# Performance work log

Measured on AMD Instinct MI355X. Metric: run time of the kernel, lower is better.

The kernel has to match this reference:

```python
import jax, jax.numpy as jnp
import numpy as np

D_MODEL = 1024
NUM_HEADS = 16
SCALE = 1.0 / np.sqrt(D_MODEL // NUM_HEADS)  # matches sqrt(d_model // num_heads)


def setup_inputs() -> dict:
    key = jax.random.key(0)
    ks = jax.random.split(key, 7)
    B, S, D = 4, 2048, D_MODEL
    std = 1.0 / np.sqrt(D)
    return {
        "x": jax.random.normal(ks[0], (B, S, D), dtype=jnp.float32),
        "Wq": jax.random.normal(ks[1], (D, D), dtype=jnp.float32) * std,
        "bq": jnp.zeros((D,), dtype=jnp.float32),
        "Wk": jax.random.normal(ks[2], (D, D), dtype=jnp.float32) * std,
        "bk": jnp.zeros((D,), dtype=jnp.float32),
        "Wv": jax.random.normal(ks[3], (D, D), dtype=jnp.float32) * std,
        "bv": jnp.zeros((D,), dtype=jnp.float32),
    }


def reference(x, Wq, bq, Wk, bk, Wv, bv):
    # QKV projections (nn.Linear: x @ W^T + b; here W stored as [in, out] already)
    Q = x @ Wq + bq  # [B, S, D]
    K = x @ Wk + bk
    V = x @ Wv + bv
    scores = jnp.einsum("bsd,btd->bst", Q, K) * SCALE  # [B, S, S]
    S_len = x.shape[1]
    causal = jnp.tril(jnp.ones((S_len, S_len), dtype=bool))
    scores = jnp.where(causal, scores, -jnp.inf)
    attn = jax.nn.softmax(scores, axis=-1)
    return jnp.einsum("bst,btd->bsd", attn, V)
```

## Files before the change

kernel.cpp:

```cpp
#include <hip/hip_runtime.h>
#include <hip/hip_bf16.h>
#include <cstdint>

#define D_MODEL 1024
#define SEQ     2048
#define SCALE   0.125f
#define P_ELEMS 2228224

typedef __attribute__((ext_vector_type(8))) _Float16 f16x8;
typedef __attribute__((ext_vector_type(8))) unsigned short u16x8;
typedef __attribute__((ext_vector_type(4))) float f32x4;

__device__ __forceinline__ unsigned short f2h(float f) {
  _Float16 h = (_Float16)f;
  return __builtin_bit_cast(unsigned short, h);
}
__device__ __forceinline__ float h2f(unsigned short u) {
  return (float)__builtin_bit_cast(_Float16, u);
}

__device__ __forceinline__ void gll16(const void* g, void* lds_p) {
  __builtin_amdgcn_global_load_lds(
      (const __attribute__((address_space(1))) unsigned int*)(uintptr_t)g,
      (__attribute__((address_space(3))) unsigned int*)(unsigned int)(uintptr_t)lds_p,
      16, 0, 0);
}

#define WAITV8 asm volatile("s_waitcnt vmcnt(8)" ::: "memory")
#define WAITV0 asm volatile("s_waitcnt vmcnt(0)" ::: "memory")
#define WAITL8 asm volatile("s_waitcnt lgkmcnt(8)" ::: "memory")
#define WAITL0 asm volatile("s_waitcnt lgkmcnt(0)" ::: "memory")
#define SCHEDB __builtin_amdgcn_sched_barrier(0)
#define BAR    __builtin_amdgcn_s_barrier()
#define PRIO1  __builtin_amdgcn_s_setprio(1)
#define PRIO0  __builtin_amdgcn_s_setprio(0)
#define MFMA16(a, b, c) __builtin_amdgcn_mfma_f32_16x16x32_f16(a, b, c, 0, 0, 0)

__device__ __forceinline__ void stage_tile(const unsigned short* gA, const unsigned short* gB,
                                           size_t sA, size_t sB,
                                           int k0, unsigned short* buf, int w, int lane) {
  int rl = lane >> 3;
  int sg = ((lane & 7) ^ rl) << 3;
#pragma unroll
  for (int j = 0; j < 4; j++) {
    int c = w * 4 + j;
    int row = c * 8 + rl;
    gll16(gA + (size_t)row * sA + k0 + sg, buf + c * 512);
    gll16(gB + (size_t)row * sB + k0 + sg, buf + 8192 + c * 512);
  }
}

__device__ __forceinline__ void gemm_core(const unsigned short* gA, const unsigned short* gB,
                                          size_t sA, size_t sB,
                                          unsigned short* lds0, unsigned short* lds1, int nt,
                                          int w, int lane, int wr, int wc, int l15, int l4,
                                          f32x4 acc[4][4]) {
  stage_tile(gA, gB, sA, sB, 0, lds0, w, lane);
  stage_tile(gA, gB, sA, sB, 64, lds1, w, lane);
  WAITV8; SCHEDB; BAR;
  for (int t = 0; t < nt; t++) {
    const unsigned short* buf = (t & 1) ? lds1 : lds0;
    const unsigned short* bA = buf;
    const unsigned short* bB = buf + 8192;
    f16x8 a0[4], b0[4], a1[4], b1[4];
#pragma unroll
    for (int m = 0; m < 4; m++) {
      int row = wr * 64 + m * 16 + l15, rs = row & 7;
      a0[m] = *(const f16x8*)(bA + row * 64 + ((l4 ^ rs) << 3));
    }
#pragma unroll
    for (int n = 0; n < 4; n++) {
      int row = wc * 64 + n * 16 + l15, rs = row & 7;
      b0[n] = *(const f16x8*)(bB + row * 64 + ((l4 ^ rs) << 3));
    }
#pragma unroll
    for (int m = 0; m < 4; m++) {
      int row = wr * 64 + m * 16 + l15, rs = row & 7;
      a1[m] = *(const f16x8*)(bA + row * 64 + (((4 + l4) ^ rs) << 3));
    }
#pragma unroll
    for (int n = 0; n < 4; n++) {
      int row = wc * 64 + n * 16 + l15, rs = row & 7;
      b1[n] = *(const f16x8*)(bB + row * 64 + (((4 + l4) ^ rs) << 3));
    }
    WAITL8; SCHEDB;
    PRIO1;
#pragma unroll
    for (int m = 0; m < 4; m++)
#pragma unroll
      for (int n = 0; n < 4; n++)
        acc[m][n] = MFMA16(a0[m], b0[n], acc[m][n]);
    PRIO0;
    WAITL0; SCHEDB; BAR;
    if (t + 2 < nt) stage_tile(gA, gB, sA, sB, (t + 2) * 64,
                               (unsigned short*)buf, w, lane);
    PRIO1;
#pragma unroll
    for (int m = 0; m < 4; m++)
#pragma unroll
      for (int n = 0; n < 4; n++)
        acc[m][n] = MFMA16(a1[m], b1[n], acc[m][n]);
    PRIO0;
    if (t + 2 < nt) { WAITV8; } else { WAITV0; }
    SCHEDB; BAR;
  }
}

__global__ __launch_bounds__(256) void cvt_fused(const float* __restrict__ x,
                                                 const float* __restrict__ W0,
                                                 const float* __restrict__ W1,
                                                 const float* __restrict__ W2,
                                                 unsigned short* __restrict__ xb,
                                                 unsigned short* __restrict__ wt) {
  __shared__ float t[32][33];
  int bid = blockIdx.x;
  int tid = threadIdx.x;
  if (bid < 4096) {
    int i = bid * 256 + tid;
    const float4* p = (const float4*)x + (size_t)i * 2;
    float4 a = p[0], b = p[1];
    u16x8 r;
    r[0] = f2h(a.x); r[1] = f2h(a.y); r[2] = f2h(a.z); r[3] = f2h(a.w);
    r[4] = f2h(b.x); r[5] = f2h(b.y); r[6] = f2h(b.z); r[7] = f2h(b.w);
    *((u16x8*)xb + i) = r;
  } else {
    int id = bid - 4096;
    int z = id >> 10, rem = id & 1023;
    int bx = rem & 31, by = rem >> 5;
    const float* W = (z == 0) ? W0 : (z == 1 ? W1 : W2);
    unsigned short* o = wt + (size_t)z * 1048576;
    int c0 = bx * 32, r0 = by * 32;
    int tx = tid & 31, ty = tid >> 5;
    for (int i = 0; i < 4; i++)
      t[ty + 8 * i][tx] = W[(size_t)(r0 + ty + 8 * i) * 1024 + c0 + tx];
    __syncthreads();
    for (int i = 0; i < 4; i++)
      o[(size_t)(c0 + ty + 8 * i) * 1024 + r0 + tx] = f2h(t[tx][ty + 8 * i]);
  }
}

__global__ __launch_bounds__(256) void qkv_gemm(const unsigned short* __restrict__ xb,
                                                const unsigned short* __restrict__ wt,
                                                const float* __restrict__ b0,
                                                const float* __restrict__ b1,
                                                const float* __restrict__ b2,
                                                unsigned short* __restrict__ Qp,
                                                unsigned short* __restrict__ Kp,
                                                unsigned short* __restrict__ vtp) {
  __shared__ unsigned short lds[2][16384];
  int m0 = blockIdx.x * 128;
  int n0 = blockIdx.y * 128;
  int z = n0 >> 10, nz = n0 & 1023;
  const unsigned short* gA = xb + (size_t)m0 * 1024;
  const unsigned short* gB = wt + (size_t)z * 1048576 + (size_t)nz * 1024;
  const float* bias = (z == 0) ? b0 : (z == 1 ? b1 : b2);
  int tid = threadIdx.x, lane = tid & 63, w = tid >> 6;
  int wr = w >> 1, wc = w & 1, l15 = lane & 15, l4 = lane >> 4;
  f32x4 acc[4][4] = {};
  gemm_core(gA, gB, 1024, 1024, &lds[0][0], &lds[1][0], 16, w, lane, wr, wc, l15, l4, acc);

  unsigned short* T = &lds[0][0];
  if (z < 2) {
    unsigned short* O = (z == 0) ? Qp : Kp;
#pragma unroll
    for (int m = 0; m < 4; m++)
#pragma unroll
      for (int n = 0; n < 4; n++) {
        int cl = wc * 64 + n * 16 + l15;
        float bv = bias[nz + cl];
#pragma unroll
        for (int r = 0; r < 4; r++) {
          int rl = wr * 64 + m * 16 + l4 * 4 + r;
          T[rl * 136 + cl] = f2h(acc[m][n][r] + bv);
        }
      }
    __syncthreads();
#pragma unroll
    for (int i = 0; i < 8; i++) {
      int idx = i * 256 + tid;
      int row = idx >> 4, ch = idx & 15;
      u16x8 v = *(const u16x8*)(T + row * 136 + ch * 8);
      *(u16x8*)(O + (size_t)(m0 + row) * 1024 + nz + ch * 8) = v;
    }
  } else {
#pragma unroll
    for (int m = 0; m < 4; m++)
#pragma unroll
      for (int n = 0; n < 4; n++) {
        int cl = wc * 64 + n * 16 + l15;
        float bv = bias[nz + cl];
#pragma unroll
        for (int r = 0; r < 4; r++) {
          int rl = wr * 64 + m * 16 + l4 * 4 + r;
          T[cl * 136 + rl] = f2h(acc[m][n][r] + bv);
        }
      }
    __syncthreads();
    int bidx = m0 >> 11, s0 = m0 & 2047;
#pragma unroll
    for (int i = 0; i < 8; i++) {
      int d = w * 32 + i * 4 + (lane >> 4);
      int ch = lane & 15;
      u16x8 v = *(const u16x8*)(T + d * 136 + ch * 8);
      *(u16x8*)(vtp + ((size_t)bidx * 1024 + nz + d) * 2048 + s0 + ch * 8) = v;
    }
  }
}

__global__ __launch_bounds__(256) void qk_scores(const unsigned short* __restrict__ Q,
                                                 const unsigned short* __restrict__ Kb,
                                                 unsigned short* __restrict__ sc) {
  __shared__ unsigned short lds[2][16384];
  int blk = blockIdx.x;
  int t0, ntile;
  if (blk < 32) { t0 = 480 + blk; ntile = 2; }
  else          { t0 = blk - 32;  ntile = 1; }
  int tid = threadIdx.x, lane = tid & 63, w = tid >> 6;
  int wr = w >> 1, wc = w & 1, l15 = lane & 15, l4 = lane >> 4;
  for (int u = 0; u < ntile; u++) {
    int ti = t0 + u * 32;
    int b = ti / 136, i = ti % 136;
    int qt = (int)((sqrtf(8.f * i + 1.f) - 1.f) * 0.5f);
    while ((qt + 1) * (qt + 2) / 2 <= i) qt++;
    while (qt * (qt + 1) / 2 > i) qt--;
    int kt = i - qt * (qt + 1) / 2;
    int Wspan = (qt + 1) << 7;
    const unsigned short* gA = Q  + ((size_t)b * 2048 + qt * 128) * 1024;
    const unsigned short* gB = Kb + ((size_t)b * 2048 + kt * 128) * 1024;
    unsigned short* outp = sc + (size_t)b * P_ELEMS + (size_t)16384 * (qt * (qt + 1) / 2);
    f32x4 acc[4][4] = {};
    gemm_core(gA, gB, 1024, 1024, &lds[0][0], &lds[1][0], 16, w, lane, wr, wc, l15, l4, acc);
    unsigned short* T = &lds[0][0];
#pragma unroll
    for (int m = 0; m < 4; m++)
#pragma unroll
      for (int n = 0; n < 4; n++) {
        int cl = wc * 64 + n * 16 + l15;
        int kv = kt * 128 + cl;
#pragma unroll
        for (int r = 0; r < 4; r++) {
          int rl = wr * 64 + m * 16 + l4 * 4 + r;
          int srow = qt * 128 + rl;
          float v = acc[m][n][r] * SCALE;
          if (kv > srow) v = -30000.f;
          T[rl * 136 + cl] = f2h(v);
        }
      }
    __syncthreads();
#pragma unroll
    for (int i2 = 0; i2 < 8; i2++) {
      int idx = i2 * 256 + tid;
      int row = idx >> 4, ch = idx & 15;
      u16x8 v = *(const u16x8*)(T + row * 136 + ch * 8);
      *(u16x8*)(outp + (size_t)row * Wspan + kt * 128 + ch * 8) = v;
    }
    __syncthreads();
  }
}

__global__ __launch_bounds__(256) void softmax_row(const unsigned short* __restrict__ sc,
                                                   unsigned short* __restrict__ pb) {
  int base = blockIdx.x * 4;
  int b = base >> 11, sl0 = base & 2047;
  int w = threadIdx.x >> 6, lane = threadIdx.x & 63;
  int sl = sl0 + w;
  int qt = sl >> 7;
  int Wspan = (qt + 1) << 7;
  size_t rb = (size_t)b * P_ELEMS + (size_t)16384 * (qt * (qt + 1) / 2) + (size_t)(sl & 127) * Wspan;
  const u16x8* src = (const u16x8*)(sc + rb);
  int nc = Wspan >> 3;
  bool h0 = lane < nc, h1 = lane + 64 < nc, h2 = lane + 128 < nc, h3 = lane + 192 < nc;
  float v0[8], v1[8], v2[8], v3[8];
  float mx = -1e30f;
  if (h0) { u16x8 r = src[lane];
#pragma unroll
    for (int j = 0; j < 8; j++) { v0[j] = h2f(r[j]); mx = fmaxf(mx, v0[j]); } }
  if (h1) { u16x8 r = src[lane + 64];
#pragma unroll
    for (int j = 0; j < 8; j++) { v1[j] = h2f(r[j]); mx = fmaxf(mx, v1[j]); } }
  if (h2) { u16x8 r = src[lane + 128];
#pragma unroll
    for (int j = 0; j < 8; j++) { v2[j] = h2f(r[j]); mx = fmaxf(mx, v2[j]); } }
  if (h3) { u16x8 r = src[lane + 192];
#pragma unroll
    for (int j = 0; j < 8; j++) { v3[j] = h2f(r[j]); mx = fmaxf(mx, v3[j]); } }
  for (int off = 1; off < 64; off <<= 1) mx = fmaxf(mx, __shfl_xor(mx, off, 64));
  float s = 0.f;
  if (h0) {
#pragma unroll
    for (int j = 0; j < 8; j++) { v0[j] = __expf(v0[j] - mx); s += v0[j]; } }
  if (h1) {
#pragma unroll
    for (int j = 0; j < 8; j++) { v1[j] = __expf(v1[j] - mx); s += v1[j]; } }
  if (h2) {
#pragma unroll
    for (int j = 0; j < 8; j++) { v2[j] = __expf(v2[j] - mx); s += v2[j]; } }
  if (h3) {
#pragma unroll
    for (int j = 0; j < 8; j++) { v3[j] = __expf(v3[j] - mx); s += v3[j]; } }
  for (int off = 1; off < 64; off <<= 1) s += __shfl_xor(s, off, 64);
  float inv = 1.f / s;
  u16x8* dst = (u16x8*)(pb + rb);
  if (h0) { u16x8 o;
#pragma unroll
    for (int j = 0; j < 8; j++) o[j] = f2h(v0[j] * inv);
    dst[lane] = o; }
  if (h1) { u16x8 o;
#pragma unroll
    for (int j = 0; j < 8; j++) o[j] = f2h(v1[j] * inv);
    dst[lane + 64] = o; }
  if (h2) { u16x8 o;
#pragma unroll
    for (int j = 0; j < 8; j++) o[j] = f2h(v2[j] * inv);
    dst[lane + 128] = o; }
  if (h3) { u16x8 o;
#pragma unroll
    for (int j = 0; j < 8; j++) o[j] = f2h(v3[j] * inv);
    dst[lane + 192] = o; }
}

__global__ __launch_bounds__(256) void pv_gemm(const unsigned short* __restrict__ pb,
                                               const unsigned short* __restrict__ vtp,
                                               float* __restrict__ outp) {
  __shared__ unsigned short lds[2][16384];
  int bx = blockIdx.x;
  int n0 = blockIdx.y * 128;
  int bz = blockIdx.z;
  int qt = (bz & 2) ? (15 - bx) : bx;
  int b = bz;
  int tid = threadIdx.x, lane = tid & 63, w = tid >> 6;
  int wr = w >> 1, wc = w & 1, l15 = lane & 15, l4 = lane >> 4;
  const unsigned short* gB = vtp + (size_t)b * 1024 * 2048 + (size_t)n0 * 2048;
  int Wspan = (qt + 1) << 7;
  const unsigned short* gA = pb + (size_t)b * P_ELEMS + (size_t)16384 * (qt * (qt + 1) / 2);
  float* O = outp + ((size_t)b * 2048 + qt * 128) * 1024;
  f32x4 acc[4][4] = {};
  gemm_core(gA, gB, Wspan, 2048, &lds[0][0], &lds[1][0], 2 * (qt + 1),
            w, lane, wr, wc, l15, l4, acc);
  float* Tf = (float*)&lds[0][0];
#pragma unroll
  for (int m = 0; m < 4; m++)
#pragma unroll
    for (int n = 0; n < 4; n++) {
      int cl = wc * 64 + n * 16 + l15;
#pragma unroll
      for (int r = 0; r < 4; r++) {
        int rl = wr * 64 + m * 16 + l4 * 4 + r;
        int cc = cl >> 2;
        int sw = (((cc ^ (rl & 7)) << 2) | (cl & 3));
        Tf[rl * 128 + sw] = acc[m][n][r];
      }
    }
  __syncthreads();
#pragma unroll
  for (int i = 0; i < 16; i++) {
    int idx = i * 256 + tid;
    int row = idx >> 5, ch = idx & 31;
    float4 val = *(const float4*)&Tf[row * 128 + ((ch ^ (row & 7)) << 2)];
    *(float4*)&O[(size_t)row * 1024 + n0 + ch * 4] = val;
  }
}

extern "C" void kernel_launch(void* const* d_in, const int* in_sizes, int n_in,
                              void* d_out, int out_size, void* d_ws, size_t ws_size,
                              hipStream_t stream) {
  const float* x  = (const float*)d_in[0];
  const float* Wq = (const float*)d_in[1];
  const float* bq = (const float*)d_in[2];
  const float* Wk = (const float*)d_in[3];
  const float* bk = (const float*)d_in[4];
  const float* Wv = (const float*)d_in[5];
  const float* bv = (const float*)d_in[6];
  float* out = (float*)d_out;

  unsigned short* ws  = (unsigned short*)d_ws;
  unsigned short* wt  = ws;
  unsigned short* Qp  = ws + 3145728;
  unsigned short* Kp  = ws + 11534336;
  unsigned short* vtp = ws + 19922944;
  unsigned short* sc  = ws + 28311552;
  unsigned short* pb  = ws + 37224448;
  unsigned short* xb  = (unsigned short*)d_out;

  cvt_fused<<<7168, 256, 0, stream>>>(x, Wq, Wk, Wv, xb, wt);
  qkv_gemm<<<dim3(64, 24), 256, 0, stream>>>(xb, wt, bq, bk, bv, Qp, Kp, vtp);
  qk_scores<<<512, 256, 0, stream>>>(Qp, Kp, sc);
  softmax_row<<<2048, 256, 0, stream>>>(sc, pb);
  pv_gemm<<<dim3(16, 8, 4), 256, 0, stream>>>(pb, vtp, out);
}
```

Baseline: 149.7 us.

## Switch GEMMs to 32x32x16 MFMA and fuse V projection into scores kernel

Replaces the 16x16x32 MFMA tiles with 32x32x16 MFMA in the shared GEMM core, so each wave issues fewer, larger matrix instructions and needs fewer LDS fragment loads per k-step. It also moves the V projection out of the QKV GEMM into the scores kernel as extra blocks. The scores tiles and the V projection tiles then run concurrently, which should fill the machine better and removes one launch-level dependency. The accumulator row mapping changes for the new MFMA layout, which risks register pressure and different epilogue bank conflicts.

```diff
diff --git a/kernel.cpp b/kernel.cpp
--- a/kernel.cpp
+++ b/kernel.cpp
@@ -9,7 +9,7 @@
 
 typedef __attribute__((ext_vector_type(8))) _Float16 f16x8;
 typedef __attribute__((ext_vector_type(8))) unsigned short u16x8;
-typedef __attribute__((ext_vector_type(4))) float f32x4;
+typedef __attribute__((ext_vector_type(16))) float f32x16;
 
 __device__ __forceinline__ unsigned short f2h(float f) {
   _Float16 h = (_Float16)f;
@@ -34,7 +34,7 @@
 #define BAR    __builtin_amdgcn_s_barrier()
 #define PRIO1  __builtin_amdgcn_s_setprio(1)
 #define PRIO0  __builtin_amdgcn_s_setprio(0)
-#define MFMA16(a, b, c) __builtin_amdgcn_mfma_f32_16x16x32_f16(a, b, c, 0, 0, 0)
+#define MFMA32(a, b, c) __builtin_amdgcn_mfma_f32_32x32x16_f16(a, b, c, 0, 0, 0)
 
 __device__ __forceinline__ void stage_tile(const unsigned short* gA, const unsigned short* gB,
                                            size_t sA, size_t sB,
@@ -52,59 +52,65 @@
 
 __device__ __forceinline__ void gemm_core(const unsigned short* gA, const unsigned short* gB,
                                           size_t sA, size_t sB,
-                                          unsigned short* lds0, unsigned short* lds1, int nt,
-                                          int w, int lane, int wr, int wc, int l15, int l4,
-                                          f32x4 acc[4][4]) {
+                                          unsigned short* lds0, unsigned short* lds1, int ntk,
+                                          int w, int lane, int wr, int wc, int l31, int l5,
+                                          f32x16 acc[2][2]) {
   stage_tile(gA, gB, sA, sB, 0, lds0, w, lane);
   stage_tile(gA, gB, sA, sB, 64, lds1, w, lane);
   WAITV8; SCHEDB; BAR;
-  for (int t = 0; t < nt; t++) {
-    const unsigned short* buf = (t & 1) ? lds1 : lds0;
+  int rA0 = wr * 64 + l31,      qA0 = rA0 & 7;
+  int rA1 = wr * 64 + 32 + l31, qA1 = rA1 & 7;
+  int rB0 = wc * 64 + l31,      qB0 = rB0 & 7;
+  int rB1 = wc * 64 + 32 + l31, qB1 = rB1 & 7;
+  for (int t = 0; t < ntk; t++) {
+    unsigned short* buf = (t & 1) ? lds1 : lds0;
     const unsigned short* bA = buf;
     const unsigned short* bB = buf + 8192;
-    f16x8 a0[4], b0[4], a1[4], b1[4];
-#pragma unroll
-    for (int m = 0; m < 4; m++) {
-      int row = wr * 64 + m * 16 + l15, rs = row & 7;
-      a0[m] = *(const f16x8*)(bA + row * 64 + ((l4 ^ rs) << 3));
-    }
-#pragma unroll
-    for (int n = 0; n < 4; n++) {
-      int row = wc * 64 + n * 16 + l15, rs = row & 7;
-      b0[n] = *(const f16x8*)(bB + row * 64 + ((l4 ^ rs) << 3));
-    }
-#pragma unroll
-    for (int m = 0; m < 4; m++) {
-      int row = wr * 64 + m * 16 + l15, rs = row & 7;
-      a1[m] = *(const f16x8*)(bA + row * 64 + (((4 + l4) ^ rs) << 3));
-    }
-#pragma unroll
-    for (int n = 0; n < 4; n++) {
-      int row = wc * 64 + n * 16 + l15, rs = row & 7;
-      b1[n] = *(const f16x8*)(bB + row * 64 + (((4 + l4) ^ rs) << 3));
+    f16x8 a[2][4], b[2][4];
+#pragma unroll
+    for (int ks = 0; ks < 2; ks++) {
+      int s = (ks << 1) | l5;
+      a[0][ks] = *(const f16x8*)(bA + rA0 * 64 + ((s ^ qA0) << 3));
+      a[1][ks] = *(const f16x8*)(bA + rA1 * 64 + ((s ^ qA1) << 3));
+      b[0][ks] = *(const f16x8*)(bB + rB0 * 64 + ((s ^ qB0) << 3));
+      b[1][ks] = *(const f16x8*)(bB + rB1 * 64 + ((s ^ qB1) << 3));
+    }
+    SCHEDB;
+#pragma unroll
+    for (int ks = 2; ks < 4; ks++) {
+      int s = (ks << 1) | l5;
+      a[0][ks] = *(const f16x8*)(bA + rA0 * 64 + ((s ^ qA0) << 3));
+      a[1][ks] = *(const f16x8*)(bA + rA1 * 64 + ((s ^ qA1) << 3));
+      b[0][ks] = *(const f16x8*)(bB + rB0 * 64 + ((s ^ qB0) << 3));
+      b[1][ks] = *(const f16x8*)(bB + rB1 * 64 + ((s ^ qB1) << 3));
     }
     WAITL8; SCHEDB;
     PRIO1;
 #pragma unroll
-    for (int m = 0; m < 4; m++)
-#pragma unroll
-      for (int n = 0; n < 4; n++)
-        acc[m][n] = MFMA16(a0[m], b0[n], acc[m][n]);
+    for (int ks = 0; ks < 2; ks++)
+#pragma unroll
+      for (int mt = 0; mt < 2; mt++)
+#pragma unroll
+        for (int nq = 0; nq < 2; nq++)
+          acc[mt][nq] = MFMA32(a[mt][ks], b[nq][ks], acc[mt][nq]);
     PRIO0;
     WAITL0; SCHEDB; BAR;
-    if (t + 2 < nt) stage_tile(gA, gB, sA, sB, (t + 2) * 64,
-                               (unsigned short*)buf, w, lane);
+    if (t + 2 < ntk) stage_tile(gA, gB, sA, sB, (t + 2) * 64, buf, w, lane);
     PRIO1;
 #pragma unroll
-    for (int m = 0; m < 4; m++)
-#pragma unroll
-      for (int n = 0; n < 4; n++)
-        acc[m][n] = MFMA16(a1[m], b1[n], acc[m][n]);
+    for (int ks = 2; ks < 4; ks++)
+#pragma unroll
+      for (int mt = 0; mt < 2; mt++)
+#pragma unroll
+        for (int nq = 0; nq < 2; nq++)
+          acc[mt][nq] = MFMA32(a[mt][ks], b[nq][ks], acc[mt][nq]);
     PRIO0;
-    if (t + 2 < nt) { WAITV8; } else { WAITV0; }
+    if (t + 2 < ntk) { WAITV8; } else { WAITV0; }
     SCHEDB; BAR;
   }
 }
+
+#define ACC_ROW(r, l5) (((r) & 3) + (((r) >> 2) << 3) + ((l5) << 2))
 
 __global__ __launch_bounds__(256) void cvt_fused(const float* __restrict__ x,
                                                  const float* __restrict__ W0,
@@ -143,56 +149,117 @@
                                                 const unsigned short* __restrict__ wt,
                                                 const float* __restrict__ b0,
                                                 const float* __restrict__ b1,
-                                                const float* __restrict__ b2,
                                                 unsigned short* __restrict__ Qp,
-                                                unsigned short* __restrict__ Kp,
-                                                unsigned short* __restrict__ vtp) {
+                                                unsigned short* __restrict__ Kp) {
   __shared__ unsigned short lds[2][16384];
   int m0 = blockIdx.x * 128;
   int n0 = blockIdx.y * 128;
   int z = n0 >> 10, nz = n0 & 1023;
   const unsigned short* gA = xb + (size_t)m0 * 1024;
   const unsigned short* gB = wt + (size_t)z * 1048576 + (size_t)nz * 1024;
-  const float* bias = (z == 0) ? b0 : (z == 1 ? b1 : b2);
+  const float* bias = z ? b1 : b0;
+  unsigned short* O = z ? Kp : Qp;
   int tid = threadIdx.x, lane = tid & 63, w = tid >> 6;
-  int wr = w >> 1, wc = w & 1, l15 = lane & 15, l4 = lane >> 4;
-  f32x4 acc[4][4] = {};
-  gemm_core(gA, gB, 1024, 1024, &lds[0][0], &lds[1][0], 16, w, lane, wr, wc, l15, l4, acc);
+  int wr = w >> 1, wc = w & 1, l31 = lane & 31, l5 = lane >> 5;
+  f32x16 acc[2][2] = {};
+  gemm_core(gA, gB, 1024, 1024, &lds[0][0], &lds[1][0], 16, w, lane, wr, wc, l31, l5, acc);
 
   unsigned short* T = &lds[0][0];
-  if (z < 2) {
-    unsigned short* O = (z == 0) ? Qp : Kp;
-#pragma unroll
-    for (int m = 0; m < 4; m++)
-#pragma unroll
-      for (int n = 0; n < 4; n++) {
-        int cl = wc * 64 + n * 16 + l15;
-        float bv = bias[nz + cl];
-#pragma unroll
-        for (int r = 0; r < 4; r++) {
-          int rl = wr * 64 + m * 16 + l4 * 4 + r;
-          T[rl * 136 + cl] = f2h(acc[m][n][r] + bv);
+#pragma unroll
+  for (int mt = 0; mt < 2; mt++)
+#pragma unroll
+    for (int nq = 0; nq < 2; nq++) {
+      int cl = wc * 64 + nq * 32 + l31;
+      float bvv = bias[nz + cl];
+#pragma unroll
+      for (int r = 0; r < 16; r++) {
+        int rl = wr * 64 + mt * 32 + ACC_ROW(r, l5);
+        T[rl * 136 + cl] = f2h(acc[mt][nq][r] + bvv);
+      }
+    }
+  __syncthreads();
+#pragma unroll
+  for (int i = 0; i < 8; i++) {
+    int idx = i * 256 + tid;
+    int row = idx >> 4, ch = idx & 15;
+    u16x8 v = *(const u16x8*)(T + row * 136 + ch * 8);
+    *(u16x8*)(O + (size_t)(m0 + row) * 1024 + nz + ch * 8) = v;
+  }
+}
+
+__global__ __launch_bounds__(256) void scores_v(const unsigned short* __restrict__ Q,
+                                                const unsigned short* __restrict__ Kb,
+                                                const unsigned short* __restrict__ xb,
+                                                const unsigned short* __restrict__ wt,
+                                                const float* __restrict__ bvf,
+                                                unsigned short* __restrict__ sc,
+                                                unsigned short* __restrict__ vtp) {
+  __shared__ unsigned short lds[2][16384];
+  int blk = blockIdx.x;
+  int tid = threadIdx.x, lane = tid & 63, w = tid >> 6;
+  int wr = w >> 1, wc = w & 1, l31 = lane & 31, l5 = lane >> 5;
+  if (blk < 512) {
+    int t0, ntile;
+    if (blk < 32) { t0 = 480 + blk; ntile = 2; }
+    else          { t0 = blk - 32;  ntile = 1; }
+    for (int u = 0; u < ntile; u++) {
+      int ti = t0 + u * 32;
+      int b = ti / 136, i = ti % 136;
+      int qt = (int)((sqrtf(8.f * i + 1.f) - 1.f) * 0.5f);
+      while ((qt + 1) * (qt + 2) / 2 <= i) qt++;
+      while (qt * (qt + 1) / 2 > i) qt--;
+      int kt = i - qt * (qt + 1) / 2;
+      int Wspan = (qt + 1) << 7;
+      const unsigned short* gA = Q  + ((size_t)b * 2048 + qt * 128) * 1024;
+      const unsigned short* gB = Kb + ((size_t)b * 2048 + kt * 128) * 1024;
+      unsigned short* outp = sc + (size_t)b * P_ELEMS + (size_t)16384 * (qt * (qt + 1) / 2);
+      f32x16 acc[2][2] = {};
+      gemm_core(gA, gB, 1024, 1024, &lds[0][0], &lds[1][0], 16, w, lane, wr, wc, l31, l5, acc);
+      unsigned short* T = &lds[0][0];
+#pragma unroll
+      for (int mt = 0; mt < 2; mt++)
+#pragma unroll
+        for (int nq = 0; nq < 2; nq++) {
+          int cl = wc * 64 + nq * 32 + l31;
+          int kv = kt * 128 + cl;
+#pragma unroll
+          for (int r = 0; r < 16; r++) {
+            int rl = wr * 64 + mt * 32 + ACC_ROW(r, l5);
+            int srow = qt * 128 + rl;
+            float v = acc[mt][nq][r] * SCALE;
+            if (kv > srow) v = -30000.f;
+            T[rl * 136 + cl] = f2h(v);
+          }
         }
+      __syncthreads();
+#pragma unroll
+      for (int i2 = 0; i2 < 8; i2++) {
+        int idx = i2 * 256 + tid;
+        int row = idx >> 4, ch = idx & 15;
+        u16x8 v = *(const u16x8*)(T + row * 136 + ch * 8);
+        *(u16x8*)(outp + (size_t)row * Wspan + kt * 128 + ch * 8) = v;
       }
-    __syncthreads();
-#pragma unroll
-    for (int i = 0; i < 8; i++) {
-      int idx = i * 256 + tid;
-      int row = idx >> 4, ch = idx & 15;
-      u16x8 v = *(const u16x8*)(T + row * 136 + ch * 8);
-      *(u16x8*)(O + (size_t)(m0 + row) * 1024 + nz + ch * 8) = v;
+      __syncthreads();
     }
   } else {
-#pragma unroll
-    for (int m = 0; m < 4; m++)
-#pragma unroll
-      for (int n = 0; n < 4; n++) {
-        int cl = wc * 64 + n * 16 + l15;
-        float bv = bias[nz + cl];
-#pragma unroll
-        for (int r = 0; r < 4; r++) {
-          int rl = wr * 64 + m * 16 + l4 * 4 + r;
-          T[cl * 136 + rl] = f2h(acc[m][n][r] + bv);
+    int id = blk - 512;
+    int m0 = (id & 63) * 128;
+    int n0v = (id >> 6) * 128;
+    const unsigned short* gA = xb + (size_t)m0 * 1024;
+    const unsigned short* gB = wt + (size_t)2 * 1048576 + (size_t)n0v * 1024;
+    f32x16 acc[2][2] = {};
+    gemm_core(gA, gB, 1024, 1024, &lds[0][0], &lds[1][0], 16, w, lane, wr, wc, l31, l5, acc);
+    unsigned short* T = &lds[0][0];
+#pragma unroll
+    for (int mt = 0; mt < 2; mt++)
+#pragma unroll
+      for (int nq = 0; nq < 2; nq++) {
+        int cl = wc * 64 + nq * 32 + l31;
+        float bvv = bvf[n0v + cl];
+#pragma unroll
+        for (int r = 0; r < 16; r++) {
+          int rl = wr * 64 + mt * 32 + ACC_ROW(r, l5);
+          T[cl * 136 + rl] = f2h(acc[mt][nq][r] + bvv);
         }
       }
     __syncthreads();
@@ -202,59 +269,8 @@
       int d = w * 32 + i * 4 + (lane >> 4);
       int ch = lane & 15;
       u16x8 v = *(const u16x8*)(T + d * 136 + ch * 8);
-      *(u16x8*)(vtp + ((size_t)bidx * 1024 + nz + d) * 2048 + s0 + ch * 8) = v;
-    }
-  }
-}
-
-__global__ __launch_bounds__(256) void qk_scores(const unsigned short* __restrict__ Q,
-                                                 const unsigned short* __restrict__ Kb,
-                                                 unsigned short* __restrict__ sc) {
-  __shared__ unsigned short lds[2][16384];
-  int blk = blockIdx.x;
-  int t0, ntile;
-  if (blk < 32) { t0 = 480 + blk; ntile = 2; }
-  else          { t0 = blk - 32;  ntile = 1; }
-  int tid = threadIdx.x, lane = tid & 63, w = tid >> 6;
-  int wr = w >> 1, wc = w & 1, l15 = lane & 15, l4 = lane >> 4;
-  for (int u = 0; u < ntile; u++) {
-    int ti = t0 + u * 32;
-    int b = ti / 136, i = ti % 136;
-    int qt = (int)((sqrtf(8.f * i + 1.f) - 1.f) * 0.5f);
-    while ((qt + 1) * (qt + 2) / 2 <= i) qt++;
-    while (qt * (qt + 1) / 2 > i) qt--;
-    int kt = i - qt * (qt + 1) / 2;
-    int Wspan = (qt + 1) << 7;
-    const unsigned short* gA = Q  + ((size_t)b * 2048 + qt * 128) * 1024;
-    const unsigned short* gB = Kb + ((size_t)b * 2048 + kt * 128) * 1024;
-    unsigned short* outp = sc + (size_t)b * P_ELEMS + (size_t)16384 * (qt * (qt + 1) / 2);
-    f32x4 acc[4][4] = {};
-    gemm_core(gA, gB, 1024, 1024, &lds[0][0], &lds[1][0], 16, w, lane, wr, wc, l15, l4, acc);
-    unsigned short* T = &lds[0][0];
-#pragma unroll
-    for (int m = 0; m < 4; m++)
-#pragma unroll
-      for (int n = 0; n < 4; n++) {
-        int cl = wc * 64 + n * 16 + l15;
-        int kv = kt * 128 + cl;
-#pragma unroll
-        for (int r = 0; r < 4; r++) {
-          int rl = wr * 64 + m * 16 + l4 * 4 + r;
-          int srow = qt * 128 + rl;
-          float v = acc[m][n][r] * SCALE;
-          if (kv > srow) v = -30000.f;
-          T[rl * 136 + cl] = f2h(v);
-        }
-      }
-    __syncthreads();
-#pragma unroll
-    for (int i2 = 0; i2 < 8; i2++) {
-      int idx = i2 * 256 + tid;
-      int row = idx >> 4, ch = idx & 15;
-      u16x8 v = *(const u16x8*)(T + row * 136 + ch * 8);
-      *(u16x8*)(outp + (size_t)row * Wspan + kt * 128 + ch * 8) = v;
-    }
-    __syncthreads();
+      *(u16x8*)(vtp + ((size_t)bidx * 1024 + n0v + d) * 2048 + s0 + ch * 8) = v;
+    }
   }
 }
 
@@ -329,26 +345,26 @@
   int qt = (bz & 2) ? (15 - bx) : bx;
   int b = bz;
   int tid = threadIdx.x, lane = tid & 63, w = tid >> 6;
-  int wr = w >> 1, wc = w & 1, l15 = lane & 15, l4 = lane >> 4;
+  int wr = w >> 1, wc = w & 1, l31 = lane & 31, l5 = lane >> 5;
   const unsigned short* gB = vtp + (size_t)b * 1024 * 2048 + (size_t)n0 * 2048;
   int Wspan = (qt + 1) << 7;
   const unsigned short* gA = pb + (size_t)b * P_ELEMS + (size_t)16384 * (qt * (qt + 1) / 2);
   float* O = outp + ((size_t)b * 2048 + qt * 128) * 1024;
-  f32x4 acc[4][4] = {};
+  f32x16 acc[2][2] = {};
   gemm_core(gA, gB, Wspan, 2048, &lds[0][0], &lds[1][0], 2 * (qt + 1),
-            w, lane, wr, wc, l15, l4, acc);
+            w, lane, wr, wc, l31, l5, acc);
   float* Tf = (float*)&lds[0][0];
 #pragma unroll
-  for (int m = 0; m < 4; m++)
-#pragma unroll
-    for (int n = 0; n < 4; n++) {
-      int cl = wc * 64 + n * 16 + l15;
-#pragma unroll
-      for (int r = 0; r < 4; r++) {
-        int rl = wr * 64 + m * 16 + l4 * 4 + r;
+  for (int mt = 0; mt < 2; mt++)
+#pragma unroll
+    for (int nq = 0; nq < 2; nq++) {
+      int cl = wc * 64 + nq * 32 + l31;
+#pragma unroll
+      for (int r = 0; r < 16; r++) {
+        int rl = wr * 64 + mt * 32 + ACC_ROW(r, l5);
         int cc = cl >> 2;
         int sw = (((cc ^ (rl & 7)) << 2) | (cl & 3));
-        Tf[rl * 128 + sw] = acc[m][n][r];
+        Tf[rl * 128 + sw] = acc[mt][nq][r];
       }
     }
   __syncthreads();
@@ -383,8 +399,8 @@
   unsigned short* xb  = (unsigned short*)d_out;
 
   cvt_fused<<<7168, 256, 0, stream>>>(x, Wq, Wk, Wv, xb, wt);
-  qkv_gemm<<<dim3(64, 24), 256, 0, stream>>>(xb, wt, bq, bk, bv, Qp, Kp, vtp);
-  qk_scores<<<512, 256, 0, stream>>>(Qp, Kp, sc);
+  qkv_gemm<<<dim3(64, 16), 256, 0, stream>>>(xb, wt, bq, bk, Qp, Kp);
+  scores_v<<<1024, 256, 0, stream>>>(Qp, Kp, xb, wt, bv, sc, vtp);
   softmax_row<<<2048, 256, 0, stream>>>(sc, pb);
   pv_gemm<<<dim3(16, 8, 4), 256, 0, stream>>>(pb, vtp, out);
 }
```

New measurement: 156.0 us. 1.04x slower.

## Move V projection into the QK-scores kernel to balance grid waves

Applied to the files above, without the earlier changes.

The V projection tiles are taken out of the QKV GEMM launch and run in the same launch as the causal QK^T score tiles, using a block-index split (first 512 blocks do scores, the next 512 compute V transposed). The QKV GEMM grid drops from 1536 to 1024 blocks and the scores kernel grows from 512 to 1024 blocks. The intent is to fill partial waves on the 256-CU device and overlap the independent V GEMM with the score GEMM, with the same total work. The combined kernel mixes two workload types, and placement of its blocks is left to the hardware scheduler.

```diff
diff --git a/kernel.cpp b/kernel.cpp
--- a/kernel.cpp
+++ b/kernel.cpp
@@ -143,56 +143,117 @@
                                                 const unsigned short* __restrict__ wt,
                                                 const float* __restrict__ b0,
                                                 const float* __restrict__ b1,
-                                                const float* __restrict__ b2,
                                                 unsigned short* __restrict__ Qp,
-                                                unsigned short* __restrict__ Kp,
-                                                unsigned short* __restrict__ vtp) {
+                                                unsigned short* __restrict__ Kp) {
   __shared__ unsigned short lds[2][16384];
   int m0 = blockIdx.x * 128;
   int n0 = blockIdx.y * 128;
   int z = n0 >> 10, nz = n0 & 1023;
   const unsigned short* gA = xb + (size_t)m0 * 1024;
   const unsigned short* gB = wt + (size_t)z * 1048576 + (size_t)nz * 1024;
-  const float* bias = (z == 0) ? b0 : (z == 1 ? b1 : b2);
+  const float* bias = z ? b1 : b0;
+  unsigned short* O = z ? Kp : Qp;
   int tid = threadIdx.x, lane = tid & 63, w = tid >> 6;
   int wr = w >> 1, wc = w & 1, l15 = lane & 15, l4 = lane >> 4;
   f32x4 acc[4][4] = {};
   gemm_core(gA, gB, 1024, 1024, &lds[0][0], &lds[1][0], 16, w, lane, wr, wc, l15, l4, acc);
 
   unsigned short* T = &lds[0][0];
-  if (z < 2) {
-    unsigned short* O = (z == 0) ? Qp : Kp;
+#pragma unroll
+  for (int m = 0; m < 4; m++)
+#pragma unroll
+    for (int n = 0; n < 4; n++) {
+      int cl = wc * 64 + n * 16 + l15;
+      float bv = bias[nz + cl];
+#pragma unroll
+      for (int r = 0; r < 4; r++) {
+        int rl = wr * 64 + m * 16 + l4 * 4 + r;
+        T[rl * 136 + cl] = f2h(acc[m][n][r] + bv);
+      }
+    }
+  __syncthreads();
+#pragma unroll
+  for (int i = 0; i < 8; i++) {
+    int idx = i * 256 + tid;
+    int row = idx >> 4, ch = idx & 15;
+    u16x8 v = *(const u16x8*)(T + row * 136 + ch * 8);
+    *(u16x8*)(O + (size_t)(m0 + row) * 1024 + nz + ch * 8) = v;
+  }
+}
+
+__global__ __launch_bounds__(256) void scores_v(const unsigned short* __restrict__ Q,
+                                                const unsigned short* __restrict__ Kb,
+                                                const unsigned short* __restrict__ xb,
+                                                const unsigned short* __restrict__ wt,
+                                                const float* __restrict__ bvf,
+                                                unsigned short* __restrict__ sc,
+                                                unsigned short* __restrict__ vtp) {
+  __shared__ unsigned short lds[2][16384];
+  int blk = blockIdx.x;
+  int tid = threadIdx.x, lane = tid & 63, w = tid >> 6;
+  int wr = w >> 1, wc = w & 1, l15 = lane & 15, l4 = lane >> 4;
+  if (blk < 512) {
+    int t0, ntile;
+    if (blk < 32) { t0 = 480 + blk; ntile = 2; }
+    else          { t0 = blk - 32;  ntile = 1; }
+    for (int u = 0; u < ntile; u++) {
+      int ti = t0 + u * 32;
+      int b = ti / 136, i = ti % 136;
+      int qt = (int)((sqrtf(8.f * i + 1.f) - 1.f) * 0.5f);
+      while ((qt + 1) * (qt + 2) / 2 <= i) qt++;
+      while (qt * (qt + 1) / 2 > i) qt--;
+      int kt = i - qt * (qt + 1) / 2;
+      int Wspan = (qt + 1) << 7;
+      const unsigned short* gA = Q  + ((size_t)b * 2048 + qt * 128) * 1024;
+      const unsigned short* gB = Kb + ((size_t)b * 2048 + kt * 128) * 1024;
+      unsigned short* outp = sc + (size_t)b * P_ELEMS + (size_t)16384 * (qt * (qt + 1) / 2);
+      f32x4 acc[4][4] = {};
+      gemm_core(gA, gB, 1024, 1024, &lds[0][0], &lds[1][0], 16, w, lane, wr, wc, l15, l4, acc);
+      unsigned short* T = &lds[0][0];
+#pragma unroll
+      for (int m = 0; m < 4; m++)
+#pragma unroll
+        for (int n = 0; n < 4; n++) {
+          int cl = wc * 64 + n * 16 + l15;
+          int kv = kt * 128 + cl;
+#pragma unroll
+          for (int r = 0; r < 4; r++) {
+            int rl = wr * 64 + m * 16 + l4 * 4 + r;
+            int srow = qt * 128 + rl;
+            float v = acc[m][n][r] * SCALE;
+            if (kv > srow) v = -30000.f;
+            T[rl * 136 + cl] = f2h(v);
+          }
+        }
+      __syncthreads();
+#pragma unroll
+      for (int i2 = 0; i2 < 8; i2++) {
+        int idx = i2 * 256 + tid;
+        int row = idx >> 4, ch = idx & 15;
+        u16x8 v = *(const u16x8*)(T + row * 136 + ch * 8);
+        *(u16x8*)(outp + (size_t)row * Wspan + kt * 128 + ch * 8) = v;
+      }
+      __syncthreads();
+    }
+  } else {
+    int id = blk - 512;
+    int m0 = (id & 63) * 128;
+    int n0v = (id >> 6) * 128;
+    const unsigned short* gA = xb + (size_t)m0 * 1024;
+    const unsigned short* gB = wt + (size_t)2 * 1048576 + (size_t)n0v * 1024;
+    f32x4 acc[4][4] = {};
+    gemm_core(gA, gB, 1024, 1024, &lds[0][0], &lds[1][0], 16, w, lane, wr, wc, l15, l4, acc);
+    unsigned short* T = &lds[0][0];
 #pragma unroll
     for (int m = 0; m < 4; m++)
 #pragma unroll
       for (int n = 0; n < 4; n++) {
         int cl = wc * 64 + n * 16 + l15;
-        float bv = bias[nz + cl];
+        float bvv = bvf[n0v + cl];
 #pragma unroll
         for (int r = 0; r < 4; r++) {
           int rl = wr * 64 + m * 16 + l4 * 4 + r;
-          T[rl * 136 + cl] = f2h(acc[m][n][r] + bv);
-        }
-      }
-    __syncthreads();
-#pragma unroll
-    for (int i = 0; i < 8; i++) {
-      int idx = i * 256 + tid;
-      int row = idx >> 4, ch = idx & 15;
-      u16x8 v = *(const u16x8*)(T + row * 136 + ch * 8);
-      *(u16x8*)(O + (size_t)(m0 + row) * 1024 + nz + ch * 8) = v;
-    }
-  } else {
-#pragma unroll
-    for (int m = 0; m < 4; m++)
-#pragma unroll
-      for (int n = 0; n < 4; n++) {
-        int cl = wc * 64 + n * 16 + l15;
-        float bv = bias[nz + cl];
-#pragma unroll
-        for (int r = 0; r < 4; r++) {
-          int rl = wr * 64 + m * 16 + l4 * 4 + r;
-          T[cl * 136 + rl] = f2h(acc[m][n][r] + bv);
+          T[cl * 136 + rl] = f2h(acc[m][n][r] + bvv);
         }
       }
     __syncthreads();
@@ -202,59 +263,8 @@
       int d = w * 32 + i * 4 + (lane >> 4);
       int ch = lane & 15;
       u16x8 v = *(const u16x8*)(T + d * 136 + ch * 8);
-      *(u16x8*)(vtp + ((size_t)bidx * 1024 + nz + d) * 2048 + s0 + ch * 8) = v;
-    }
-  }
-}
-
-__global__ __launch_bounds__(256) void qk_scores(const unsigned short* __restrict__ Q,
-                                                 const unsigned short* __restrict__ Kb,
-                                                 unsigned short* __restrict__ sc) {
-  __shared__ unsigned short lds[2][16384];
-  int blk = blockIdx.x;
-  int t0, ntile;
-  if (blk < 32) { t0 = 480 + blk; ntile = 2; }
-  else          { t0 = blk - 32;  ntile = 1; }
-  int tid = threadIdx.x, lane = tid & 63, w = tid >> 6;
-  int wr = w >> 1, wc = w & 1, l15 = lane & 15, l4 = lane >> 4;
-  for (int u = 0; u < ntile; u++) {
-    int ti = t0 + u * 32;
-    int b = ti / 136, i = ti % 136;
-    int qt = (int)((sqrtf(8.f * i + 1.f) - 1.f) * 0.5f);
-    while ((qt + 1) * (qt + 2) / 2 <= i) qt++;
-    while (qt * (qt + 1) / 2 > i) qt--;
-    int kt = i - qt * (qt + 1) / 2;
-    int Wspan = (qt + 1) << 7;
-    const unsigned short* gA = Q  + ((size_t)b * 2048 + qt * 128) * 1024;
-    const unsigned short* gB = Kb + ((size_t)b * 2048 + kt * 128) * 1024;
-    unsigned short* outp = sc + (size_t)b * P_ELEMS + (size_t)16384 * (qt * (qt + 1) / 2);
-    f32x4 acc[4][4] = {};
-    gemm_core(gA, gB, 1024, 1024, &lds[0][0], &lds[1][0], 16, w, lane, wr, wc, l15, l4, acc);
-    unsigned short* T = &lds[0][0];
-#pragma unroll
-    for (int m = 0; m < 4; m++)
-#pragma unroll
-      for (int n = 0; n < 4; n++) {
-        int cl = wc * 64 + n * 16 + l15;
-        int kv = kt * 128 + cl;
-#pragma unroll
-        for (int r = 0; r < 4; r++) {
-          int rl = wr * 64 + m * 16 + l4 * 4 + r;
-          int srow = qt * 128 + rl;
-          float v = acc[m][n][r] * SCALE;
-          if (kv > srow) v = -30000.f;
-          T[rl * 136 + cl] = f2h(v);
-        }
-      }
-    __syncthreads();
-#pragma unroll
-    for (int i2 = 0; i2 < 8; i2++) {
-      int idx = i2 * 256 + tid;
-      int row = idx >> 4, ch = idx & 15;
-      u16x8 v = *(const u16x8*)(T + row * 136 + ch * 8);
-      *(u16x8*)(outp + (size_t)row * Wspan + kt * 128 + ch * 8) = v;
-    }
-    __syncthreads();
+      *(u16x8*)(vtp + ((size_t)bidx * 1024 + n0v + d) * 2048 + s0 + ch * 8) = v;
+    }
   }
 }
 
@@ -383,8 +393,8 @@
   unsigned short* xb  = (unsigned short*)d_out;
 
   cvt_fused<<<7168, 256, 0, stream>>>(x, Wq, Wk, Wv, xb, wt);
-  qkv_gemm<<<dim3(64, 24), 256, 0, stream>>>(xb, wt, bq, bk, bv, Qp, Kp, vtp);
-  qk_scores<<<512, 256, 0, stream>>>(Qp, Kp, sc);
+  qkv_gemm<<<dim3(64, 16), 256, 0, stream>>>(xb, wt, bq, bk, Qp, Kp);
+  scores_v<<<1024, 256, 0, stream>>>(Qp, Kp, xb, wt, bv, sc, vtp);
   softmax_row<<<2048, 256, 0, stream>>>(sc, pb);
   pv_gemm<<<dim3(16, 8, 4), 256, 0, stream>>>(pb, vtp, out);
 }
```

Result: no change. 148.2 us, median of 2 (-1.1%).
